# Optimization experiments

Measured on AMD Instinct MI355X. Metric: run time of the kernel, lower is better.

The kernel has to match this reference:

```python
import jax, jax.numpy as jnp
import numpy as np
from functools import partial

T, B, I, H = 512, 64, 512, 512


def setup_inputs() -> dict:
    key = jax.random.key(0)
    ks = jax.random.split(key, 4)
    std = 0.01
    x = jax.random.normal(ks[0], (T, B, I), dtype=jnp.float32)
    a0 = jnp.zeros((B, H), dtype=jnp.float32)
    # packed gate weights, gate order: [update(u), forget(f), output(o), candidate(c)]
    W = jax.random.normal(ks[1], (I, 4 * H), dtype=jnp.float32) * std
    U = jax.random.normal(ks[2], (H, 4 * H), dtype=jnp.float32) * std
    b = jax.random.normal(ks[3], (4 * H,), dtype=jnp.float32) * std
    return {"x": x, "a0": a0, "W": W, "U": U, "b": b}


def reference(x, a0, W, U, b):
    h = a0.shape[-1]
    # precompute input projections for all timesteps: [T, B, 4H]
    xW = jnp.einsum("tbi,ig->tbg", x, W) + b

    def step(a_tm1, xw_t):
        g = xw_t + a_tm1 @ U  # [B, 4H]
        gamma_u = jax.nn.sigmoid(g[..., 0 * h:1 * h])
        gamma_f = jax.nn.sigmoid(g[..., 1 * h:2 * h])
        gamma_o = jax.nn.sigmoid(g[..., 2 * h:3 * h])
        c_tilde = jnp.tanh(g[..., 3 * h:4 * h])
        # NOTE: faithful to source — forget gate multiplies previous HIDDEN state
        c_t = gamma_u * c_tilde + gamma_f * a_tm1
        a_t = gamma_o * jnp.tanh(c_t)
        return a_t, a_t

    _, hs = jax.lax.scan(step, a0, xW)
    return hs  # [T, B, H]
```

## Files before the change

### kernel.cpp

```cpp
#include <hip/hip_runtime.h>
#include <cstddef>
#include <cstdint>


#define T_STEPS 512
#define NB      64
#define HID     512
#define G4      2048
#define KDIM    512
#define BB      4
#define NSL     32
#define BLK_DW  (NSL * 256)
#define PAR_DW  (BB * BLK_DW)

typedef short bf16x8 __attribute__((ext_vector_type(8)));
typedef float f32x4  __attribute__((ext_vector_type(4)));
typedef unsigned int u32x4 __attribute__((ext_vector_type(4)));

__device__ __forceinline__ float bf2f(unsigned short s) {
    unsigned u = ((unsigned)s) << 16;
    float f; __builtin_memcpy(&f, &u, 4); return f;
}
__device__ __forceinline__ unsigned short f2bf(float f) {
    unsigned u; __builtin_memcpy(&u, &f, 4);
    u = (u + 0x7FFFu + ((u >> 16) & 1u)) >> 16;
    return (unsigned short)u;
}
__device__ __forceinline__ unsigned min4(u32x4 v) {
    unsigned a = v[0] < v[1] ? v[0] : v[1];
    unsigned b = v[2] < v[3] ? v[2] : v[3];
    return a < b ? a : b;
}

__global__ void cast_x_kernel(const float* __restrict__ x,
                              unsigned short* __restrict__ o,
                              unsigned* __restrict__ abq) {
    if (blockIdx.x < 256)
        abq[blockIdx.x * 256 + threadIdx.x] = 0u;
    size_t i = (size_t)blockIdx.x * blockDim.x + threadIdx.x;
    float4 v = ((const float4*)x)[i];
    ushort4 r;
    r.x = f2bf(v.x); r.y = f2bf(v.y); r.z = f2bf(v.z); r.w = f2bf(v.w);
    ((ushort4*)o)[i] = r;
}

__global__ void transpose_cast(const float* __restrict__ src,
                               unsigned short* __restrict__ dst) {
    __shared__ float tile[64][65];
    const int n0 = blockIdx.x * 64;
    const int k0 = blockIdx.y * 64;
    const int c  = threadIdx.x & 63;
    const int r0 = threadIdx.x >> 6;
    for (int p = 0; p < 16; ++p) {
        int r = p * 4 + r0;
        tile[r][c] = src[(size_t)(k0 + r) * G4 + n0 + c];
    }
    __syncthreads();
    for (int p = 0; p < 16; ++p) {
        int r = p * 4 + r0;
        dst[(size_t)(n0 + r) * KDIM + k0 + c] = f2bf(tile[c][r]);
    }
}

__global__ __launch_bounds__(256) void gemm_xw(
        const unsigned short* __restrict__ A,
        const unsigned short* __restrict__ Bt,
        const float* __restrict__ bias,
        unsigned short* __restrict__ C) {
    __shared__ unsigned short As[128][56];
    __shared__ unsigned short Bs[128][56];
    const int m0 = blockIdx.x * 128;
    const int n0 = blockIdx.y * 128;
    const int tid = threadIdx.x;
    const int lane = tid & 63, wave = tid >> 6;
    const int quad = lane >> 4, l16 = lane & 15;
    const int wm = (wave >> 1) * 64, wn = (wave & 1) * 64;
    f32x4 acc[4][4];
    for (int i = 0; i < 4; ++i)
        for (int j = 0; j < 4; ++j) acc[i][j] = (f32x4)0.0f;
    const int srow = tid >> 2, scol = (tid & 3) * 8;
    for (int k0 = 0; k0 < KDIM; k0 += 32) {
        __syncthreads();
        for (int p = 0; p < 2; ++p) {
            int row = p * 64 + srow;
            *(uint4*)&As[row][scol] =
                *(const uint4*)&A[(size_t)(m0 + row) * KDIM + k0 + scol];
            *(uint4*)&Bs[row][scol] =
                *(const uint4*)&Bt[(size_t)(n0 + row) * KDIM + k0 + scol];
        }
        __syncthreads();
        bf16x8 af[4], bf[4];
        for (int i = 0; i < 4; ++i)
            af[i] = *(const bf16x8*)&As[wm + i * 16 + l16][quad * 8];
        for (int j = 0; j < 4; ++j)
            bf[j] = *(const bf16x8*)&Bs[wn + j * 16 + l16][quad * 8];
        for (int i = 0; i < 4; ++i)
            for (int j = 0; j < 4; ++j)
                acc[i][j] = __builtin_amdgcn_mfma_f32_16x16x32_bf16(
                    af[i], bf[j], acc[i][j], 0, 0, 0);
    }
    for (int i = 0; i < 4; ++i)
        for (int j = 0; j < 4; ++j) {
            int col = n0 + wn + j * 16 + l16;
            int g   = col >> 9;
            int u   = col & 511;
            int js  = u >> 4, ut = u & 15;
            float bv = bias[col];
            for (int r = 0; r < 4; ++r) {
                int row = m0 + wm + i * 16 + quad * 4 + r;
                int t = row >> 6, b = row & 63;
                size_t off = ((((size_t)t * BB + (b >> 4)) * NSL + js) * 4 + g)
                                 * 256 + (b & 15) * 16 + ut;
                C[off] = f2bf(acc[i][j][r] + bv);
            }
        }
}

__global__ __launch_bounds__(256) void lstm_rec(
        const unsigned short* __restrict__ xWp,
        const unsigned short* __restrict__ Ut,
        const float* __restrict__ a0,
        float* __restrict__ out,
        unsigned* __restrict__ abq) {
    __shared__ unsigned short a_lds[16][520];
    __shared__ float gbuf[4][16][20];
    const int wgid  = blockIdx.x;
    const int i_blk = wgid >> 5;
    const int j_sl  = wgid & 31;
    const int tid   = threadIdx.x;
    const int wave  = tid >> 6;
    const int lane  = tid & 63;
    const int quad  = lane >> 4, l16 = lane & 15;
    const int j0 = j_sl * 16;
    const int b0 = i_blk * 16;
    const int bt = tid >> 4;
    const int ut = tid & 15;

    bf16x8 bq[16];
    {
        const unsigned short* urow =
            Ut + (size_t)(wave * HID + j0 + l16) * KDIM + quad * 8;
        for (int s = 0; s < 16; ++s)
            bq[s] = *(const bf16x8*)(urow + s * 32);
    }
    float aown = a0[(size_t)(b0 + bt) * HID + j0 + ut];
    __hip_atomic_store(
        &abq[(size_t)i_blk * BLK_DW + j_sl * 256 + tid],
        (unsigned)f2bf(aown) | (1u << 16),
        __ATOMIC_RELAXED, __HIP_MEMORY_SCOPE_AGENT);

    unsigned short xsA[4], xsB[4];
    {
        const unsigned short* xp =
            xWp + ((size_t)i_blk * NSL + j_sl) * 1024;
#pragma unroll
        for (int w = 0; w < 4; ++w)
            xsA[w] = __builtin_nontemporal_load(&xp[w * 256 + tid]);
    }

    auto step = [&](int t, unsigned short* xs, unsigned short* xsn) {
        const unsigned* srcblk =
            abq + (size_t)(t & 1) * PAR_DW + (size_t)i_blk * BLK_DW;
        const u32x4* pc = (const u32x4*)srcblk + tid;
        const unsigned w16 = (unsigned)(t + 1) << 16;
        u32x4 d0, d1, d2, d3, d4, d5, d6, d7;
        bool okf;
        do {
            asm volatile(
                "global_load_dwordx4 %0, %8, off sc1\n\t"
                "global_load_dwordx4 %1, %9, off sc1\n\t"
                "global_load_dwordx4 %2, %10, off sc1\n\t"
                "global_load_dwordx4 %3, %11, off sc1\n\t"
                "global_load_dwordx4 %4, %12, off sc1\n\t"
                "global_load_dwordx4 %5, %13, off sc1\n\t"
                "global_load_dwordx4 %6, %14, off sc1\n\t"
                "global_load_dwordx4 %7, %15, off sc1\n\t"
                "s_waitcnt vmcnt(0)"
                : "=&v"(d0), "=&v"(d1), "=&v"(d2), "=&v"(d3),
                  "=&v"(d4), "=&v"(d5), "=&v"(d6), "=&v"(d7)
                : "v"(pc),        "v"(pc + 256),  "v"(pc + 512),
                  "v"(pc + 768),  "v"(pc + 1024), "v"(pc + 1280),
                  "v"(pc + 1536), "v"(pc + 1792)
                : "memory");
            unsigned m01 = min4(d0) < min4(d1) ? min4(d0) : min4(d1);
            unsigned m23 = min4(d2) < min4(d3) ? min4(d2) : min4(d3);
            unsigned m45 = min4(d4) < min4(d5) ? min4(d4) : min4(d5);
            unsigned m67 = min4(d6) < min4(d7) ? min4(d6) : min4(d7);
            unsigned ma = m01 < m23 ? m01 : m23;
            unsigned mb = m45 < m67 ? m45 : m67;
            okf = ((ma < mb ? ma : mb) >= w16);
        } while (!okf);

        {
            int tn = (t + 1 < T_STEPS) ? t + 1 : t;
            const unsigned short* xp =
                xWp + (((size_t)tn * BB + i_blk) * NSL + j_sl) * 1024;
#pragma unroll
            for (int w = 0; w < 4; ++w)
                xsn[w] = __builtin_nontemporal_load(&xp[w * 256 + tid]);
        }

#define SCAT(q, d)                                                          \
        {                                                                   \
            int c = (q) * 256 + tid;                                        \
            unsigned lo = ((d)[0] & 0xffffu) | ((d)[1] << 16);              \
            unsigned hi = ((d)[2] & 0xffffu) | ((d)[3] << 16);              \
            uint2 pk; pk.x = lo; pk.y = hi;                                 \
            *(uint2*)&a_lds[(c >> 2) & 15][(c >> 6) * 16 + (c & 3) * 4] = pk;\
        }
        SCAT(0, d0) SCAT(1, d1) SCAT(2, d2) SCAT(3, d3)
        SCAT(4, d4) SCAT(5, d5) SCAT(6, d6) SCAT(7, d7)
#undef SCAT
        __syncthreads();

        f32x4 acc0 = (f32x4)0.0f, acc1 = (f32x4)0.0f;
        f32x4 acc2 = (f32x4)0.0f, acc3 = (f32x4)0.0f;
#pragma unroll
        for (int s = 0; s < 16; s += 4) {
            bf16x8 af0 = *(const bf16x8*)&a_lds[l16][(s + 0) * 32 + quad * 8];
            bf16x8 af1 = *(const bf16x8*)&a_lds[l16][(s + 1) * 32 + quad * 8];
            bf16x8 af2 = *(const bf16x8*)&a_lds[l16][(s + 2) * 32 + quad * 8];
            bf16x8 af3 = *(const bf16x8*)&a_lds[l16][(s + 3) * 32 + quad * 8];
            acc0 = __builtin_amdgcn_mfma_f32_16x16x32_bf16(af0, bq[s + 0], acc0, 0, 0, 0);
            acc1 = __builtin_amdgcn_mfma_f32_16x16x32_bf16(af1, bq[s + 1], acc1, 0, 0, 0);
            acc2 = __builtin_amdgcn_mfma_f32_16x16x32_bf16(af2, bq[s + 2], acc2, 0, 0, 0);
            acc3 = __builtin_amdgcn_mfma_f32_16x16x32_bf16(af3, bq[s + 3], acc3, 0, 0, 0);
        }
#pragma unroll
        for (int r = 0; r < 4; ++r)
            gbuf[wave][quad * 4 + r][l16] =
                (acc0[r] + acc1[r]) + (acc2[r] + acc3[r]);
        __syncthreads();

        {
            float gu = gbuf[0][bt][ut] + bf2f(xs[0]);
            float gf = gbuf[1][bt][ut] + bf2f(xs[1]);
            float go = gbuf[2][bt][ut] + bf2f(xs[2]);
            float gc = gbuf[3][bt][ut] + bf2f(xs[3]);
            float su = 1.f / (1.f + __expf(-gu));
            float sf = 1.f / (1.f + __expf(-gf));
            float so = 1.f / (1.f + __expf(-go));
            float e2 = __expf(2.f * gc);
            float tc = 1.f - 2.f / (e2 + 1.f);
            float cc = su * tc + sf * aown;
            float ec = __expf(2.f * cc);
            float th = 1.f - 2.f / (ec + 1.f);
            float a  = so * th;
            aown = a;
            __hip_atomic_store(
                &abq[(size_t)((t + 1) & 1) * PAR_DW + (size_t)i_blk * BLK_DW +
                     j_sl * 256 + tid],
                (unsigned)f2bf(a) | ((unsigned)(t + 2) << 16),
                __ATOMIC_RELAXED, __HIP_MEMORY_SCOPE_AGENT);
            __builtin_nontemporal_store(
                a, &out[((size_t)t * NB + b0 + bt) * HID + j0 + ut]);
        }
    };

    for (int t = 0; t < T_STEPS; t += 2) {
        step(t,     xsA, xsB);
        step(t + 1, xsB, xsA);
    }
}

extern "C" void kernel_launch(void* const* d_in, const int* in_sizes, int n_in,
                              void* d_out, int out_size, void* d_ws, size_t ws_size,
                              hipStream_t stream) {
    (void)in_sizes; (void)n_in; (void)out_size; (void)ws_size;
    const float* x    = (const float*)d_in[0];
    const float* a0   = (const float*)d_in[1];
    const float* W    = (const float*)d_in[2];
    const float* U    = (const float*)d_in[3];
    const float* bias = (const float*)d_in[4];
    float* out = (float*)d_out;

    char* ws = (char*)d_ws;
    unsigned short* xbf  = (unsigned short*)(ws);
    unsigned short* Wt   = (unsigned short*)(ws + 33554432);
    unsigned short* Ut   = (unsigned short*)(ws + 35651584);
    unsigned short* xWp  = (unsigned short*)(ws + 37748736);
    unsigned*       abq  = (unsigned*)(ws + 171966464);

    cast_x_kernel<<<16384, 256, 0, stream>>>(x, xbf, abq);
    transpose_cast<<<dim3(32, 8), 256, 0, stream>>>(W, Wt);
    transpose_cast<<<dim3(32, 8), 256, 0, stream>>>(U, Ut);
    gemm_xw<<<dim3(256, 16), 256, 0, stream>>>(xbf, Wt, bias, xWp);
    lstm_rec<<<BB * NSL, 256, 0, stream>>>(xWp, Ut, a0, out, abq);
}
```

Measured before the change: 1.452 ms.

## Retile recurrent LSTM workgroups to 8 batch x 32 hidden and poll with sc0

Changes the recurrent kernel partition from 16 batch rows x 16 hidden units per workgroup to 8 batch rows x 32 hidden units. Each workgroup now polls half as much of the shared hidden-state exchange buffer per step (4 loads instead of 8) and issues two MFMA column tiles per wave. Polling first uses sc0 loads and falls back to sc1 after repeated misses. The new-state stores are duplicated at workgroup and agent scope, and the nontemporal loads and stores become ordinary ones. Half of each MFMA A tile is zero padding, so some matrix work is wasted, and the visibility of sc0 polling across compute units is uncertain.

```diff
diff --git a/kernel.cpp b/kernel.cpp
--- a/kernel.cpp
+++ b/kernel.cpp
@@ -8,8 +8,8 @@
 #define HID     512
 #define G4      2048
 #define KDIM    512
-#define BB      4
-#define NSL     32
+#define BB      8
+#define NSL     16
 #define BLK_DW  (NSL * 256)
 #define PAR_DW  (BB * BLK_DW)
 
@@ -104,50 +104,58 @@
             int col = n0 + wn + j * 16 + l16;
             int g   = col >> 9;
             int u   = col & 511;
-            int js  = u >> 4, ut = u & 15;
+            int js  = u >> 5, utl = u & 31;
             float bv = bias[col];
             for (int r = 0; r < 4; ++r) {
                 int row = m0 + wm + i * 16 + quad * 4 + r;
                 int t = row >> 6, b = row & 63;
-                size_t off = ((((size_t)t * BB + (b >> 4)) * NSL + js) * 4 + g)
-                                 * 256 + (b & 15) * 16 + ut;
+                size_t off = ((((size_t)t * BB + (b >> 3)) * NSL + js) * 4 + g)
+                                 * 256 + (b & 7) * 32 + utl;
                 C[off] = f2bf(acc[i][j][r] + bv);
             }
         }
 }
 
-__global__ __launch_bounds__(256) void lstm_rec(
+__global__ __launch_bounds__(256, 1) void lstm_rec(
         const unsigned short* __restrict__ xWp,
         const unsigned short* __restrict__ Ut,
         const float* __restrict__ a0,
         float* __restrict__ out,
         unsigned* __restrict__ abq) {
     __shared__ unsigned short a_lds[16][520];
-    __shared__ float gbuf[4][16][20];
+    __shared__ float gbuf[4][8][36];
     const int wgid  = blockIdx.x;
-    const int i_blk = wgid >> 5;
-    const int j_sl  = wgid & 31;
+    const int i_blk = wgid & 7;
+    const int j_sl  = wgid >> 3;
     const int tid   = threadIdx.x;
     const int wave  = tid >> 6;
     const int lane  = tid & 63;
     const int quad  = lane >> 4, l16 = lane & 15;
-    const int j0 = j_sl * 16;
-    const int b0 = i_blk * 16;
-    const int bt = tid >> 4;
-    const int ut = tid & 15;
-
-    bf16x8 bq[16];
+    const int j0 = j_sl * 32;
+    const int b0 = i_blk * 8;
+    const int bt = tid >> 5;
+    const int ut = tid & 31;
+
+    for (int i = tid; i < 2080; i += 256)
+        ((unsigned*)&a_lds[8][0])[i] = 0u;
+
+    bf16x8 bq[2][16];
+#pragma unroll
+    for (int n = 0; n < 2; ++n) {
+        const unsigned short* urow =
+            Ut + (size_t)(wave * HID + j0 + n * 16 + l16) * KDIM + quad * 8;
+#pragma unroll
+        for (int s = 0; s < 16; ++s)
+            bq[n][s] = *(const bf16x8*)(urow + s * 32);
+    }
+
+    float aown = a0[(size_t)(b0 + bt) * HID + j0 + ut];
     {
-        const unsigned short* urow =
-            Ut + (size_t)(wave * HID + j0 + l16) * KDIM + quad * 8;
-        for (int s = 0; s < 16; ++s)
-            bq[s] = *(const bf16x8*)(urow + s * 32);
-    }
-    float aown = a0[(size_t)(b0 + bt) * HID + j0 + ut];
-    __hip_atomic_store(
-        &abq[(size_t)i_blk * BLK_DW + j_sl * 256 + tid],
-        (unsigned)f2bf(aown) | (1u << 16),
-        __ATOMIC_RELAXED, __HIP_MEMORY_SCOPE_AGENT);
+        unsigned* pp = &abq[(size_t)i_blk * BLK_DW + j_sl * 256 + tid];
+        unsigned pv = (unsigned)f2bf(aown) | (1u << 16);
+        __hip_atomic_store(pp, pv, __ATOMIC_RELAXED, __HIP_MEMORY_SCOPE_WORKGROUP);
+        __hip_atomic_store(pp, pv, __ATOMIC_RELAXED, __HIP_MEMORY_SCOPE_AGENT);
+    }
 
     unsigned short xsA[4], xsB[4];
     {
@@ -155,40 +163,37 @@
             xWp + ((size_t)i_blk * NSL + j_sl) * 1024;
 #pragma unroll
         for (int w = 0; w < 4; ++w)
-            xsA[w] = __builtin_nontemporal_load(&xp[w * 256 + tid]);
-    }
+            xsA[w] = xp[w * 256 + tid];
+    }
+
+    bool fast = true;
+
+#define LOADS(FLAG)                                                         \
+    asm volatile(                                                           \
+        "global_load_dwordx4 %0, %4, off " FLAG "\n\t"                      \
+        "global_load_dwordx4 %1, %5, off " FLAG "\n\t"                      \
+        "global_load_dwordx4 %2, %6, off " FLAG "\n\t"                      \
+        "global_load_dwordx4 %3, %7, off " FLAG "\n\t"                      \
+        "s_waitcnt vmcnt(0)"                                                \
+        : "=&v"(d0), "=&v"(d1), "=&v"(d2), "=&v"(d3)                        \
+        : "v"(pc), "v"(pc + 256), "v"(pc + 512), "v"(pc + 768)              \
+        : "memory")
 
     auto step = [&](int t, unsigned short* xs, unsigned short* xsn) {
         const unsigned* srcblk =
             abq + (size_t)(t & 1) * PAR_DW + (size_t)i_blk * BLK_DW;
         const u32x4* pc = (const u32x4*)srcblk + tid;
         const unsigned w16 = (unsigned)(t + 1) << 16;
-        u32x4 d0, d1, d2, d3, d4, d5, d6, d7;
+        u32x4 d0, d1, d2, d3;
         bool okf;
+        int tries = 0;
         do {
-            asm volatile(
-                "global_load_dwordx4 %0, %8, off sc1\n\t"
-                "global_load_dwordx4 %1, %9, off sc1\n\t"
-                "global_load_dwordx4 %2, %10, off sc1\n\t"
-                "global_load_dwordx4 %3, %11, off sc1\n\t"
-                "global_load_dwordx4 %4, %12, off sc1\n\t"
-                "global_load_dwordx4 %5, %13, off sc1\n\t"
-                "global_load_dwordx4 %6, %14, off sc1\n\t"
-                "global_load_dwordx4 %7, %15, off sc1\n\t"
-                "s_waitcnt vmcnt(0)"
-                : "=&v"(d0), "=&v"(d1), "=&v"(d2), "=&v"(d3),
-                  "=&v"(d4), "=&v"(d5), "=&v"(d6), "=&v"(d7)
-                : "v"(pc),        "v"(pc + 256),  "v"(pc + 512),
-                  "v"(pc + 768),  "v"(pc + 1024), "v"(pc + 1280),
-                  "v"(pc + 1536), "v"(pc + 1792)
-                : "memory");
+            if (__builtin_expect(fast, 1)) { LOADS("sc0"); }
+            else                           { LOADS("sc1"); }
             unsigned m01 = min4(d0) < min4(d1) ? min4(d0) : min4(d1);
             unsigned m23 = min4(d2) < min4(d3) ? min4(d2) : min4(d3);
-            unsigned m45 = min4(d4) < min4(d5) ? min4(d4) : min4(d5);
-            unsigned m67 = min4(d6) < min4(d7) ? min4(d6) : min4(d7);
-            unsigned ma = m01 < m23 ? m01 : m23;
-            unsigned mb = m45 < m67 ? m45 : m67;
-            okf = ((ma < mb ? ma : mb) >= w16);
+            okf = ((m01 < m23 ? m01 : m23) >= w16);
+            if (!okf && ++tries > 32) fast = false;
         } while (!okf);
 
         {
@@ -197,39 +202,41 @@
                 xWp + (((size_t)tn * BB + i_blk) * NSL + j_sl) * 1024;
 #pragma unroll
             for (int w = 0; w < 4; ++w)
-                xsn[w] = __builtin_nontemporal_load(&xp[w * 256 + tid]);
+                xsn[w] = xp[w * 256 + tid];
         }
 
 #define SCAT(q, d)                                                          \
         {                                                                   \
-            int c = (q) * 256 + tid;                                        \
+            int dd = ((q) << 10) + tid * 4;                                 \
+            int bb = (dd >> 5) & 7;                                         \
+            int kg = ((dd >> 8) << 5) | (dd & 31);                          \
             unsigned lo = ((d)[0] & 0xffffu) | ((d)[1] << 16);              \
             unsigned hi = ((d)[2] & 0xffffu) | ((d)[3] << 16);              \
             uint2 pk; pk.x = lo; pk.y = hi;                                 \
-            *(uint2*)&a_lds[(c >> 2) & 15][(c >> 6) * 16 + (c & 3) * 4] = pk;\
+            *(uint2*)&a_lds[bb][kg] = pk;                                   \
         }
         SCAT(0, d0) SCAT(1, d1) SCAT(2, d2) SCAT(3, d3)
-        SCAT(4, d4) SCAT(5, d5) SCAT(6, d6) SCAT(7, d7)
 #undef SCAT
         __syncthreads();
 
-        f32x4 acc0 = (f32x4)0.0f, acc1 = (f32x4)0.0f;
-        f32x4 acc2 = (f32x4)0.0f, acc3 = (f32x4)0.0f;
-#pragma unroll
-        for (int s = 0; s < 16; s += 4) {
+        f32x4 acc0a = (f32x4)0.0f, acc0b = (f32x4)0.0f;
+        f32x4 acc1a = (f32x4)0.0f, acc1b = (f32x4)0.0f;
+#pragma unroll
+        for (int s = 0; s < 16; s += 2) {
             bf16x8 af0 = *(const bf16x8*)&a_lds[l16][(s + 0) * 32 + quad * 8];
             bf16x8 af1 = *(const bf16x8*)&a_lds[l16][(s + 1) * 32 + quad * 8];
-            bf16x8 af2 = *(const bf16x8*)&a_lds[l16][(s + 2) * 32 + quad * 8];
-            bf16x8 af3 = *(const bf16x8*)&a_lds[l16][(s + 3) * 32 + quad * 8];
-            acc0 = __builtin_amdgcn_mfma_f32_16x16x32_bf16(af0, bq[s + 0], acc0, 0, 0, 0);
-            acc1 = __builtin_amdgcn_mfma_f32_16x16x32_bf16(af1, bq[s + 1], acc1, 0, 0, 0);
-            acc2 = __builtin_amdgcn_mfma_f32_16x16x32_bf16(af2, bq[s + 2], acc2, 0, 0, 0);
-            acc3 = __builtin_amdgcn_mfma_f32_16x16x32_bf16(af3, bq[s + 3], acc3, 0, 0, 0);
-        }
-#pragma unroll
-        for (int r = 0; r < 4; ++r)
-            gbuf[wave][quad * 4 + r][l16] =
-                (acc0[r] + acc1[r]) + (acc2[r] + acc3[r]);
+            acc0a = __builtin_amdgcn_mfma_f32_16x16x32_bf16(af0, bq[0][s + 0], acc0a, 0, 0, 0);
+            acc1a = __builtin_amdgcn_mfma_f32_16x16x32_bf16(af0, bq[1][s + 0], acc1a, 0, 0, 0);
+            acc0b = __builtin_amdgcn_mfma_f32_16x16x32_bf16(af1, bq[0][s + 1], acc0b, 0, 0, 0);
+            acc1b = __builtin_amdgcn_mfma_f32_16x16x32_bf16(af1, bq[1][s + 1], acc1b, 0, 0, 0);
+        }
+        if (quad < 2) {
+#pragma unroll
+            for (int r = 0; r < 4; ++r) {
+                gbuf[wave][quad * 4 + r][l16]      = acc0a[r] + acc0b[r];
+                gbuf[wave][quad * 4 + r][16 + l16] = acc1a[r] + acc1b[r];
+            }
+        }
         __syncthreads();
 
         {
@@ -247,13 +254,12 @@
             float th = 1.f - 2.f / (ec + 1.f);
             float a  = so * th;
             aown = a;
-            __hip_atomic_store(
-                &abq[(size_t)((t + 1) & 1) * PAR_DW + (size_t)i_blk * BLK_DW +
-                     j_sl * 256 + tid],
-                (unsigned)f2bf(a) | ((unsigned)(t + 2) << 16),
-                __ATOMIC_RELAXED, __HIP_MEMORY_SCOPE_AGENT);
-            __builtin_nontemporal_store(
-                a, &out[((size_t)t * NB + b0 + bt) * HID + j0 + ut]);
+            unsigned* pp = &abq[(size_t)((t + 1) & 1) * PAR_DW +
+                                (size_t)i_blk * BLK_DW + j_sl * 256 + tid];
+            unsigned pv = (unsigned)f2bf(a) | ((unsigned)(t + 2) << 16);
+            __hip_atomic_store(pp, pv, __ATOMIC_RELAXED, __HIP_MEMORY_SCOPE_WORKGROUP);
+            __hip_atomic_store(pp, pv, __ATOMIC_RELAXED, __HIP_MEMORY_SCOPE_AGENT);
+            out[((size_t)t * NB + b0 + bt) * HID + j0 + ut] = a;
         }
     };
 
@@ -261,6 +267,7 @@
         step(t,     xsA, xsB);
         step(t + 1, xsB, xsA);
     }
+#undef LOADS
 }
 
 extern "C" void kernel_launch(void* const* d_in, const int* in_sizes, int n_in,
```

Result: faster. 1.334 ms (-8.2%).
